# Kernel tuning notes

Measured on AMD Instinct MI355X. Metric: run time of the kernel, lower is better.

## Reference

```python
import jax, jax.numpy as jnp
import numpy as np

N, E = 50000, 800000
IN, EIN, HID, OUT = 128, 64, 64, 64
NEG_SLOPE = 0.2


def setup_inputs() -> dict:
    key = jax.random.key(0)
    ks = jax.random.split(key, 24)
    p = lambda k, shape: jax.random.normal(k, shape, jnp.float32) * 0.05
    return {
        'x': jax.random.normal(ks[0], (N, IN), jnp.float32),
        'edge_index': jax.random.randint(ks[1], (2, E), 0, N, jnp.int64),
        'edge_attr': jax.random.normal(ks[2], (E, EIN), jnp.float32),
        'batch': jnp.sort(jax.random.randint(ks[3], (N,), 0, 64, jnp.int64)),
        # GATConv 1 (in -> hidden, edge_dim=EIN)
        'W1': p(ks[4], (IN, HID)), 'a_src1': p(ks[5], (HID,)), 'a_dst1': p(ks[6], (HID,)),
        'We1': p(ks[7], (EIN, HID)), 'a_e1': p(ks[8], (HID,)), 'b1': jnp.zeros((HID,), jnp.float32),
        # GATConv 2 (hidden -> out)
        'W2': p(ks[9], (HID, OUT)), 'a_src2': p(ks[10], (OUT,)), 'a_dst2': p(ks[11], (OUT,)),
        'We2': p(ks[12], (EIN, OUT)), 'a_e2': p(ks[13], (OUT,)), 'b2': jnp.zeros((OUT,), jnp.float32),
        # edge MLP
        'Wm1': p(ks[14], (EIN, HID)), 'bm1': jnp.zeros((HID,), jnp.float32),
        'Wm2': p(ks[15], (HID, OUT)), 'bm2': jnp.zeros((OUT,), jnp.float32),
    }


def _gat(x, src, dst, edge_attr, W, a_s, a_d, We, a_e, b, n):
    # PyG GATConv (heads=1): add self-loops with edge_attr fill_value='mean'
    ones = jnp.ones((src.shape[0],), x.dtype)
    deg = jax.ops.segment_sum(ones, dst, num_segments=n)
    loop_attr = jax.ops.segment_sum(edge_attr, dst, num_segments=n) / jnp.maximum(deg, 1.0)[:, None]
    ar = jnp.arange(n)
    src2 = jnp.concatenate([src, ar])
    dst2 = jnp.concatenate([dst, ar])
    ea = jnp.concatenate([edge_attr, loop_attr], axis=0)  # [E+N, EIN]
    h = x @ W                                             # [N, C]
    a_src = h @ a_s                                       # [N]
    a_dst = h @ a_d                                       # [N]
    a_edge = (ea @ We) @ a_e                              # [E+N]
    alpha = jax.nn.leaky_relu(a_src[src2] + a_dst[dst2] + a_edge, NEG_SLOPE)
    # scatter-softmax over incoming edges of each dst node
    amax = jax.ops.segment_max(alpha, dst2, num_segments=n)
    ex = jnp.exp(alpha - amax[dst2])
    denom = jax.ops.segment_sum(ex, dst2, num_segments=n)
    coef = ex / denom[dst2]                               # [E+N]
    out = jax.ops.segment_sum(h[src2] * coef[:, None], dst2, num_segments=n)
    return out + b


def reference(x, edge_index, edge_attr, batch,
              W1, a_src1, a_dst1, We1, a_e1, b1,
              W2, a_src2, a_dst2, We2, a_e2, b2,
              Wm1, bm1, Wm2, bm2):
    n = x.shape[0]
    src, dst = edge_index[0], edge_index[1]
    h = _gat(x, src, dst, edge_attr, W1, a_src1, a_dst1, We1, a_e1, b1, n)
    h = jax.nn.elu(h)
    h = _gat(h, src, dst, edge_attr, W2, a_src2, a_dst2, We2, a_e2, b2, n)
    e = jax.nn.relu(edge_attr @ Wm1 + bm1) @ Wm2 + bm2
    return h, e, batch
```

## Files before the change

### kernel.cpp

```cpp
#include <hip/hip_runtime.h>

constexpr int NN = 50000;
constexpr int NE = 800000;
constexpr int C = 64;
constexpr int IN_DIM = 128;
constexpr float NEG = 0.2f;
constexpr int NB = (NN + 255) / 256;

typedef __attribute__((ext_vector_type(8))) short short8;
typedef __attribute__((ext_vector_type(4))) float f32x4;

__device__ __forceinline__ unsigned short f2bf(float f) {
    unsigned u = __float_as_uint(f);
    unsigned r = 0x7FFFu + ((u >> 16) & 1u);
    return (unsigned short)((u + r) >> 16);
}
__device__ __forceinline__ unsigned pack_bf2(float a, float b) {
    return (unsigned)f2bf(a) | ((unsigned)f2bf(b) << 16);
}

__global__ void k_vecs(const float* __restrict__ We1, const float* __restrict__ ae1v,
                       const float* __restrict__ We2, const float* __restrict__ ae2v,
                       const float* __restrict__ W1, const float* __restrict__ as1,
                       const float* __restrict__ ad1,
                       const float* __restrict__ W2, const float* __restrict__ as2,
                       const float* __restrict__ ad2,
                       float* __restrict__ out) {
    int t = blockIdx.x * blockDim.x + threadIdx.x;
    const float* M; const float* v; int row;
    if      (t < 64)  { M = We1; v = ae1v; row = t; }
    else if (t < 128) { M = We2; v = ae2v; row = t - 64; }
    else if (t < 256) { M = W1;  v = as1;  row = t - 128; }
    else if (t < 384) { M = W1;  v = ad1;  row = t - 256; }
    else if (t < 448) { M = W2;  v = as2;  row = t - 384; }
    else              { M = W2;  v = ad2;  row = t - 448; }
    float s = 0.f;
    #pragma unroll
    for (int c = 0; c < 64; ++c) s += M[row * 64 + c] * v[c];
    out[t] = s;
}

__global__ __launch_bounds__(256) void k_mlp_mfma(
        const float* __restrict__ ea,
        const float* __restrict__ Wm1, const float* __restrict__ bm1,
        const float* __restrict__ Wm2, const float* __restrict__ bm2,
        const float* __restrict__ wv,
        float* __restrict__ eout, float* __restrict__ ae1, float* __restrict__ ae2) {
    constexpr int AP = 144;
    __shared__ char Atile[128 * AP];
    __shared__ char Bt1[64 * AP];
    __shared__ char Bt2[64 * AP];
    const int t = threadIdx.x;
    const long long E0 = (long long)blockIdx.x * 128;
    const int l = t & 63;

    {
        const int j = t & 15;
        const int eb = t >> 4;
        float4 wk1 = *(const float4*)&wv[j * 4];
        float4 wk2 = *(const float4*)&wv[64 + j * 4];
        const float4* g = (const float4*)(ea + E0 * 64);
        float s1[8], s2[8];
        #pragma unroll
        for (int q = 0; q < 8; ++q) {
            float4 v = g[t + 256 * q];
            int e = eb + 16 * q;
            s1[q] = v.x * wk1.x + v.y * wk1.y + v.z * wk1.z + v.w * wk1.w;
            s2[q] = v.x * wk2.x + v.y * wk2.y + v.z * wk2.z + v.w * wk2.w;
            uint2 wr;
            wr.x = pack_bf2(v.x, v.y);
            wr.y = pack_bf2(v.z, v.w);
            *(uint2*)(Atile + e * AP + j * 8) = wr;
        }
        #pragma unroll
        for (int off = 1; off < 16; off <<= 1) {
            #pragma unroll
            for (int q = 0; q < 8; ++q) {
                s1[q] += __shfl_xor(s1[q], off);
                s2[q] += __shfl_xor(s2[q], off);
            }
        }
        float o1 = 0.f, o2 = 0.f;
        #pragma unroll
        for (int q = 0; q < 8; ++q) {
            if (j == q)     o1 = s1[q];
            if (j == q + 8) o2 = s2[q];
        }
        if (j < 8) ae1[E0 + eb + 16 * j] = o1;
        else       ae2[E0 + eb + 16 * (j - 8)] = o2;
    }
    {
        const int c = t & 63, kq = t >> 6;
        #pragma unroll
        for (int i = 0; i < 16; i += 2) {
            int k = kq * 16 + i;
            *(unsigned*)(Bt1 + c * AP + k * 2) = pack_bf2(Wm1[k * 64 + c], Wm1[(k + 1) * 64 + c]);
            *(unsigned*)(Bt2 + c * AP + k * 2) = pack_bf2(Wm2[k * 64 + c], Wm2[(k + 1) * 64 + c]);
        }
    }
    __syncthreads();

    const int m0 = (t >> 6) * 32;
    const int lr = l & 15;
    const int lk = (l >> 4) * 8;

    f32x4 acc[2][4] = {};
    #pragma unroll
    for (int ks = 0; ks < 2; ++ks) {
        int ko = ks * 32 + lk;
        short8 a0 = *(const short8*)(Atile + (m0 + lr) * AP + ko * 2);
        short8 a1 = *(const short8*)(Atile + (m0 + 16 + lr) * AP + ko * 2);
        #pragma unroll
        for (int nt = 0; nt < 4; ++nt) {
            short8 b = *(const short8*)(Bt1 + (nt * 16 + lr) * AP + ko * 2);
            acc[0][nt] = __builtin_amdgcn_mfma_f32_16x16x32_bf16(a0, b, acc[0][nt], 0, 0, 0);
            acc[1][nt] = __builtin_amdgcn_mfma_f32_16x16x32_bf16(a1, b, acc[1][nt], 0, 0, 0);
        }
    }
    {
        float b1v[4];
        #pragma unroll
        for (int nt = 0; nt < 4; ++nt) b1v[nt] = bm1[nt * 16 + lr];
        #pragma unroll
        for (int mt = 0; mt < 2; ++mt)
        #pragma unroll
        for (int nt = 0; nt < 4; ++nt)
        #pragma unroll
        for (int r = 0; r < 4; ++r) {
            int row = m0 + mt * 16 + (l >> 4) * 4 + r;
            int col = nt * 16 + lr;
            float v = fmaxf(acc[mt][nt][r] + b1v[nt], 0.f);
            *(unsigned short*)(Atile + row * AP + col * 2) = f2bf(v);
        }
    }
    f32x4 acc2[2][4] = {};
    #pragma unroll
    for (int ks = 0; ks < 2; ++ks) {
        int ko = ks * 32 + lk;
        short8 a0 = *(const short8*)(Atile + (m0 + lr) * AP + ko * 2);
        short8 a1 = *(const short8*)(Atile + (m0 + 16 + lr) * AP + ko * 2);
        #pragma unroll
        for (int nt = 0; nt < 4; ++nt) {
            short8 b = *(const short8*)(Bt2 + (nt * 16 + lr) * AP + ko * 2);
            acc2[0][nt] = __builtin_amdgcn_mfma_f32_16x16x32_bf16(a0, b, acc2[0][nt], 0, 0, 0);
            acc2[1][nt] = __builtin_amdgcn_mfma_f32_16x16x32_bf16(a1, b, acc2[1][nt], 0, 0, 0);
        }
    }
    {
        float b2v[4];
        #pragma unroll
        for (int nt = 0; nt < 4; ++nt) b2v[nt] = bm2[nt * 16 + lr];
        #pragma unroll
        for (int mt = 0; mt < 2; ++mt)
        #pragma unroll
        for (int nt = 0; nt < 4; ++nt)
        #pragma unroll
        for (int r = 0; r < 4; ++r) {
            int row = m0 + mt * 16 + (l >> 4) * 4 + r;
            eout[(E0 + row) * 64 + nt * 16 + lr] = acc2[mt][nt][r] + b2v[nt];
        }
    }
}

template <int K>
__global__ __launch_bounds__(256) void k_feat_mfma(
        const float* __restrict__ x, const float* __restrict__ W,
        const float* __restrict__ uv,
        float* __restrict__ h, float* __restrict__ asrc, float* __restrict__ adst,
        int M) {
    constexpr int AP = K * 2 + 16;
    constexpr int QW = K / 4;
    constexpr int NQ = K / 8;
    constexpr int EPQ = 256 / QW;
    __shared__ char Atile[128 * AP];
    __shared__ char Bt[64 * AP];
    const int t = threadIdx.x;
    const int M0 = blockIdx.x * 128;
    const int l = t & 63;

    {
        const int j = t % QW;
        const int eb = t / QW;
        float4 wk1 = *(const float4*)&uv[j * 4];
        float4 wk2 = *(const float4*)&uv[K + j * 4];
        const float4* g = (const float4*)(x + (long long)M0 * K);
        float s1[NQ], s2[NQ];
        #pragma unroll
        for (int q = 0; q < NQ; ++q) {
            int e = eb + EPQ * q;
            float4 v = make_float4(0.f, 0.f, 0.f, 0.f);
            if (M0 + e < M) v = g[t + 256 * q];
            s1[q] = v.x * wk1.x + v.y * wk1.y + v.z * wk1.z + v.w * wk1.w;
            s2[q] = v.x * wk2.x + v.y * wk2.y + v.z * wk2.z + v.w * wk2.w;
            uint2 wr;
            wr.x = pack_bf2(v.x, v.y);
            wr.y = pack_bf2(v.z, v.w);
            *(uint2*)(Atile + e * AP + j * 8) = wr;
        }
        #pragma unroll
        for (int off = 1; off < QW; off <<= 1) {
            #pragma unroll
            for (int q = 0; q < NQ; ++q) {
                s1[q] += __shfl_xor(s1[q], off);
                s2[q] += __shfl_xor(s2[q], off);
            }
        }
        float o1 = 0.f, o2 = 0.f;
        #pragma unroll
        for (int q = 0; q < NQ; ++q) {
            if (j == q)      o1 = s1[q];
            if (j == q + NQ) o2 = s2[q];
        }
        if (j < NQ) { int e = eb + EPQ * j;        if (M0 + e < M) asrc[M0 + e] = o1; }
        else        { int e = eb + EPQ * (j - NQ); if (M0 + e < M) adst[M0 + e] = o2; }
    }
    {
        const int c = t & 63, kq = t >> 6;
        #pragma unroll
        for (int i = 0; i < K / 4; i += 2) {
            int k = kq * (K / 4) + i;
            *(unsigned*)(Bt + c * AP + k * 2) = pack_bf2(W[k * 64 + c], W[(k + 1) * 64 + c]);
        }
    }
    __syncthreads();

    const int m0 = (t >> 6) * 32;
    const int lr = l & 15;
    const int lk = (l >> 4) * 8;

    f32x4 acc[2][4] = {};
    #pragma unroll
    for (int ks = 0; ks < K / 32; ++ks) {
        int ko = ks * 32 + lk;
        short8 a0 = *(const short8*)(Atile + (m0 + lr) * AP + ko * 2);
        short8 a1 = *(const short8*)(Atile + (m0 + 16 + lr) * AP + ko * 2);
        #pragma unroll
        for (int nt = 0; nt < 4; ++nt) {
            short8 b = *(const short8*)(Bt + (nt * 16 + lr) * AP + ko * 2);
            acc[0][nt] = __builtin_amdgcn_mfma_f32_16x16x32_bf16(a0, b, acc[0][nt], 0, 0, 0);
            acc[1][nt] = __builtin_amdgcn_mfma_f32_16x16x32_bf16(a1, b, acc[1][nt], 0, 0, 0);
        }
    }
    #pragma unroll
    for (int mt = 0; mt < 2; ++mt)
    #pragma unroll
    for (int nt = 0; nt < 4; ++nt)
    #pragma unroll
    for (int r = 0; r < 4; ++r) {
        int row = m0 + mt * 16 + (l >> 4) * 4 + r;
        if (M0 + row < M)
            h[(long long)(M0 + row) * 64 + nt * 16 + lr] = acc[mt][nt][r];
    }
}

__global__ void k_hist(const int* __restrict__ dst, int* __restrict__ hist) {
    int t = blockIdx.x * blockDim.x + threadIdx.x;
    if (t >= NE) return;
    atomicAdd(&hist[dst[t]], 1);
}

__global__ void k_scan1(const int* __restrict__ hist, int* __restrict__ row_ptr,
                        int* __restrict__ bsum) {
    __shared__ int s[256];
    int t = threadIdx.x;
    int idx = blockIdx.x * 256 + t;
    int v = (idx < NN) ? hist[idx] : 0;
    s[t] = v;
    __syncthreads();
    #pragma unroll
    for (int off = 1; off < 256; off <<= 1) {
        int x = (t >= off) ? s[t - off] : 0;
        __syncthreads();
        s[t] += x;
        __syncthreads();
    }
    if (idx < NN) row_ptr[idx] = s[t] - v;
    if (t == 255) bsum[blockIdx.x] = s[255];
}

__global__ void k_scan2(int* __restrict__ bsum) {
    __shared__ int s[256];
    int t = threadIdx.x;
    int v = (t < NB) ? bsum[t] : 0;
    s[t] = v;
    __syncthreads();
    #pragma unroll
    for (int off = 1; off < 256; off <<= 1) {
        int x = (t >= off) ? s[t - off] : 0;
        __syncthreads();
        s[t] += x;
        __syncthreads();
    }
    if (t < NB) bsum[t] = s[t] - v;
}

__global__ void k_scan3(const int* __restrict__ bsum, int* __restrict__ row_ptr,
                        int* __restrict__ cursor) {
    int idx = blockIdx.x * 256 + threadIdx.x;
    if (idx < NN) {
        int r = row_ptr[idx] + bsum[blockIdx.x];
        row_ptr[idx] = r;
        cursor[idx] = r;
    }
    if (idx == 0) row_ptr[NN] = NE;
}

__global__ void k_scatter(const int* __restrict__ src, const int* __restrict__ dst,
                          const float* __restrict__ ae1, const float* __restrict__ ae2,
                          int* __restrict__ cursor, float4* __restrict__ csr) {
    int t = blockIdx.x * blockDim.x + threadIdx.x;
    if (t >= NE) return;
    int d = dst[t];
    int pos = atomicAdd(&cursor[d], 1);
    csr[pos] = make_float4(__int_as_float(src[t]), ae1[t], ae2[t], 0.f);
}

template <bool IS_L1>
__global__ void k_gat(const int* __restrict__ row_ptr, const float4* __restrict__ csr,
                      const float* __restrict__ asrc, const float* __restrict__ adst,
                      const float* __restrict__ h, const float* __restrict__ bias,
                      float* __restrict__ out) {
    int n = blockIdx.x * 4 + (threadIdx.x >> 6);
    if (n >= NN) return;
    int lane = threadIdx.x & 63;
    int g = lane >> 4, s = lane & 15;
    int beg = row_ptr[n], end = row_ptr[n + 1];
    float adn = adst[n];
    float m = -1e30f, l = 0.f, sum_ae = 0.f;
    float4 acc = make_float4(0.f, 0.f, 0.f, 0.f);

    int i = beg + g;
    float4 rc = make_float4(0.f, 0.f, 0.f, 0.f);
    float4 hv = rc;
    float asv = 0.f;
    if (i < end) {
        rc = csr[i];
        int sr = __float_as_int(rc.x);
        hv = *(const float4*)&h[(long long)sr * 64 + s * 4];
        asv = asrc[sr];
    }
    for (; i < end; i += 4) {
        float4 rn = rc, hn = hv; float asn = asv;
        if (i + 4 < end) {
            rn = csr[i + 4];
            int sr2 = __float_as_int(rn.x);
            hn = *(const float4*)&h[(long long)sr2 * 64 + s * 4];
            asn = asrc[sr2];
        }
        float ae = IS_L1 ? rc.y : rc.z;
        sum_ae += ae;
        float a = asv + adn + ae;
        a = a > 0.f ? a : NEG * a;
        float mn = fmaxf(m, a);
        float sc = __expf(m - mn), p = __expf(a - mn);
        l = l * sc + p;
        acc.x = acc.x * sc + p * hv.x;
        acc.y = acc.y * sc + p * hv.y;
        acc.z = acc.z * sc + p * hv.z;
        acc.w = acc.w * sc + p * hv.w;
        m = mn;
        rc = rn; hv = hn; asv = asn;
    }
    #pragma unroll
    for (int off = 16; off < 64; off <<= 1) {
        float mo = __shfl_xor(m, off);
        float lo = __shfl_xor(l, off);
        float ax = __shfl_xor(acc.x, off);
        float ay = __shfl_xor(acc.y, off);
        float az = __shfl_xor(acc.z, off);
        float aw = __shfl_xor(acc.w, off);
        float so = __shfl_xor(sum_ae, off);
        float mn = fmaxf(m, mo);
        float s1 = __expf(m - mn), s2 = __expf(mo - mn);
        l = l * s1 + lo * s2;
        acc.x = acc.x * s1 + ax * s2;
        acc.y = acc.y * s1 + ay * s2;
        acc.z = acc.z * s1 + az * s2;
        acc.w = acc.w * s1 + aw * s2;
        sum_ae += so;
        m = mn;
    }
    {
        float deg = (float)(end - beg);
        float ae = sum_ae / fmaxf(deg, 1.f);
        float a = asrc[n] + adn + ae;
        a = a > 0.f ? a : NEG * a;
        float4 hvn = *(const float4*)&h[(long long)n * 64 + s * 4];
        float mn = fmaxf(m, a);
        float sc = __expf(m - mn), p = __expf(a - mn);
        l = l * sc + p;
        acc.x = acc.x * sc + p * hvn.x;
        acc.y = acc.y * sc + p * hvn.y;
        acc.z = acc.z * sc + p * hvn.z;
        acc.w = acc.w * sc + p * hvn.w;
    }
    if (g == 0) {
        float4 o;
        o.x = acc.x / l + bias[s * 4 + 0];
        o.y = acc.y / l + bias[s * 4 + 1];
        o.z = acc.z / l + bias[s * 4 + 2];
        o.w = acc.w / l + bias[s * 4 + 3];
        if (IS_L1) {
            o.x = o.x > 0.f ? o.x : expm1f(o.x);
            o.y = o.y > 0.f ? o.y : expm1f(o.y);
            o.z = o.z > 0.f ? o.z : expm1f(o.z);
            o.w = o.w > 0.f ? o.w : expm1f(o.w);
        }
        *(float4*)&out[(long long)n * 64 + s * 4] = o;
    }
}

__global__ void k_batch(const int* __restrict__ batch, float* __restrict__ out) {
    int t = blockIdx.x * blockDim.x + threadIdx.x;
    if (t >= NN) return;
    out[t] = (float)batch[t];
}

extern "C" void kernel_launch(void* const* d_in, const int* in_sizes, int n_in,
                              void* d_out, int out_size, void* d_ws, size_t ws_size,
                              hipStream_t stream) {
    const float* x     = (const float*)d_in[0];
    const int*   eidx  = (const int*)d_in[1];
    const float* eattr = (const float*)d_in[2];
    const int*   batch = (const int*)d_in[3];
    const float* W1 = (const float*)d_in[4];
    const float* as1 = (const float*)d_in[5];
    const float* ad1 = (const float*)d_in[6];
    const float* We1 = (const float*)d_in[7];
    const float* vae1 = (const float*)d_in[8];
    const float* b1  = (const float*)d_in[9];
    const float* W2 = (const float*)d_in[10];
    const float* as2 = (const float*)d_in[11];
    const float* ad2 = (const float*)d_in[12];
    const float* We2 = (const float*)d_in[13];
    const float* vae2 = (const float*)d_in[14];
    const float* b2  = (const float*)d_in[15];
    const float* Wm1 = (const float*)d_in[16];
    const float* bm1 = (const float*)d_in[17];
    const float* Wm2 = (const float*)d_in[18];
    const float* bm2 = (const float*)d_in[19];

    const int* src = eidx;
    const int* dst = eidx + NE;

    float* out_h = (float*)d_out;
    float* out_e = out_h + (long long)NN * C;
    float* out_b = out_e + (long long)NE * C;

    float4* csr   = (float4*)d_ws;
    float* ae1    = (float*)(csr + NE);
    float* ae2    = ae1 + NE;
    float* h      = ae2 + NE;
    float* out1   = h + (long long)NN * C;
    float* asrc   = out1 + (long long)NN * C;
    float* adst   = asrc + NN;
    float* vecs   = adst + NN;
    int*   hist   = (int*)(vecs + 512);
    int*   row_ptr= hist + NN;
    int*   cursor = row_ptr + NN + 1;
    int*   bsum   = cursor + NN;

    k_vecs<<<2, 256, 0, stream>>>(We1, vae1, We2, vae2, W1, as1, ad1, W2, as2, ad2, vecs);

    k_mlp_mfma<<<NE / 128, 256, 0, stream>>>(eattr, Wm1, bm1, Wm2, bm2, vecs,
                                             out_e, ae1, ae2);

    (void)hipMemsetAsync(hist, 0, sizeof(int) * NN, stream);
    k_hist<<<(NE + 255) / 256, 256, 0, stream>>>(dst, hist);
    k_scan1<<<NB, 256, 0, stream>>>(hist, row_ptr, bsum);
    k_scan2<<<1, 256, 0, stream>>>(bsum);
    k_scan3<<<NB, 256, 0, stream>>>(bsum, row_ptr, cursor);
    k_scatter<<<(NE + 255) / 256, 256, 0, stream>>>(src, dst, ae1, ae2, cursor, csr);

    k_feat_mfma<IN_DIM><<<(NN + 127) / 128, 256, 0, stream>>>(x, W1, vecs + 128,
                                                              h, asrc, adst, NN);
    k_gat<true><<<(NN + 3) / 4, 256, 0, stream>>>(row_ptr, csr, asrc, adst, h, b1, out1);

    k_feat_mfma<C><<<(NN + 127) / 128, 256, 0, stream>>>(out1, W2, vecs + 384,
                                                         h, asrc, adst, NN);
    k_gat<false><<<(NN + 3) / 4, 256, 0, stream>>>(row_ptr, csr, asrc, adst, h, b2, out_h);

    k_batch<<<(NN + 255) / 256, 256, 0, stream>>>(batch, out_b);
}
```

Before: 304.9 us.

## Store node features and CSR edge scores in bf16, fuse histogram into MLP

```diff
diff --git a/kernel.cpp b/kernel.cpp
--- a/kernel.cpp
+++ b/kernel.cpp
@@ -17,6 +17,9 @@
 }
 __device__ __forceinline__ unsigned pack_bf2(float a, float b) {
     return (unsigned)f2bf(a) | ((unsigned)f2bf(b) << 16);
+}
+__device__ __forceinline__ float bf2f(unsigned u) {
+    return __uint_as_float(u << 16);
 }
 
 __global__ void k_vecs(const float* __restrict__ We1, const float* __restrict__ ae1v,
@@ -41,11 +44,12 @@
 }
 
 __global__ __launch_bounds__(256) void k_mlp_mfma(
-        const float* __restrict__ ea,
+        const float* __restrict__ ea, const int* __restrict__ dst,
         const float* __restrict__ Wm1, const float* __restrict__ bm1,
         const float* __restrict__ Wm2, const float* __restrict__ bm2,
         const float* __restrict__ wv,
-        float* __restrict__ eout, float* __restrict__ ae1, float* __restrict__ ae2) {
+        float* __restrict__ eout, float* __restrict__ ae1, float* __restrict__ ae2,
+        int* __restrict__ hist) {
     constexpr int AP = 144;
     __shared__ char Atile[128 * AP];
     __shared__ char Bt1[64 * AP];
@@ -53,6 +57,8 @@
     const int t = threadIdx.x;
     const long long E0 = (long long)blockIdx.x * 128;
     const int l = t & 63;
+
+    if (t < 128) atomicAdd(&hist[dst[E0 + t]], 1);
 
     {
         const int j = t & 15;
@@ -166,8 +172,8 @@
 __global__ __launch_bounds__(256) void k_feat_mfma(
         const float* __restrict__ x, const float* __restrict__ W,
         const float* __restrict__ uv,
-        float* __restrict__ h, float* __restrict__ asrc, float* __restrict__ adst,
-        int M) {
+        unsigned short* __restrict__ h, float* __restrict__ asrc,
+        float* __restrict__ adst, int M) {
     constexpr int AP = K * 2 + 16;
     constexpr int QW = K / 4;
     constexpr int NQ = K / 8;
@@ -249,14 +255,8 @@
     for (int r = 0; r < 4; ++r) {
         int row = m0 + mt * 16 + (l >> 4) * 4 + r;
         if (M0 + row < M)
-            h[(long long)(M0 + row) * 64 + nt * 16 + lr] = acc[mt][nt][r];
-    }
-}
-
-__global__ void k_hist(const int* __restrict__ dst, int* __restrict__ hist) {
-    int t = blockIdx.x * blockDim.x + threadIdx.x;
-    if (t >= NE) return;
-    atomicAdd(&hist[dst[t]], 1);
+            h[(long long)(M0 + row) * 64 + nt * 16 + lr] = f2bf(acc[mt][nt][r]);
+    }
 }
 
 __global__ void k_scan1(const int* __restrict__ hist, int* __restrict__ row_ptr,
@@ -307,18 +307,18 @@
 
 __global__ void k_scatter(const int* __restrict__ src, const int* __restrict__ dst,
                           const float* __restrict__ ae1, const float* __restrict__ ae2,
-                          int* __restrict__ cursor, float4* __restrict__ csr) {
+                          int* __restrict__ cursor, uint2* __restrict__ csr) {
     int t = blockIdx.x * blockDim.x + threadIdx.x;
     if (t >= NE) return;
     int d = dst[t];
     int pos = atomicAdd(&cursor[d], 1);
-    csr[pos] = make_float4(__int_as_float(src[t]), ae1[t], ae2[t], 0.f);
+    csr[pos] = make_uint2((unsigned)src[t], pack_bf2(ae1[t], ae2[t]));
 }
 
 template <bool IS_L1>
-__global__ void k_gat(const int* __restrict__ row_ptr, const float4* __restrict__ csr,
+__global__ void k_gat(const int* __restrict__ row_ptr, const uint2* __restrict__ csr,
                       const float* __restrict__ asrc, const float* __restrict__ adst,
-                      const float* __restrict__ h, const float* __restrict__ bias,
+                      const unsigned short* __restrict__ h, const float* __restrict__ bias,
                       float* __restrict__ out) {
     int n = blockIdx.x * 4 + (threadIdx.x >> 6);
     if (n >= NN) return;
@@ -330,36 +330,34 @@
     float4 acc = make_float4(0.f, 0.f, 0.f, 0.f);
 
     int i = beg + g;
-    float4 rc = make_float4(0.f, 0.f, 0.f, 0.f);
-    float4 hv = rc;
+    uint2 rc = make_uint2(0u, 0u);
+    ushort4 hu = make_ushort4(0, 0, 0, 0);
     float asv = 0.f;
     if (i < end) {
         rc = csr[i];
-        int sr = __float_as_int(rc.x);
-        hv = *(const float4*)&h[(long long)sr * 64 + s * 4];
-        asv = asrc[sr];
+        hu = *(const ushort4*)&h[(long long)rc.x * 64 + s * 4];
+        asv = asrc[rc.x];
     }
     for (; i < end; i += 4) {
-        float4 rn = rc, hn = hv; float asn = asv;
+        uint2 rn = rc; ushort4 hn = hu; float asn = asv;
         if (i + 4 < end) {
             rn = csr[i + 4];
-            int sr2 = __float_as_int(rn.x);
-            hn = *(const float4*)&h[(long long)sr2 * 64 + s * 4];
-            asn = asrc[sr2];
-        }
-        float ae = IS_L1 ? rc.y : rc.z;
+            hn = *(const ushort4*)&h[(long long)rn.x * 64 + s * 4];
+            asn = asrc[rn.x];
+        }
+        float ae = IS_L1 ? bf2f(rc.y & 0xFFFFu) : bf2f(rc.y >> 16);
         sum_ae += ae;
         float a = asv + adn + ae;
         a = a > 0.f ? a : NEG * a;
         float mn = fmaxf(m, a);
         float sc = __expf(m - mn), p = __expf(a - mn);
         l = l * sc + p;
-        acc.x = acc.x * sc + p * hv.x;
-        acc.y = acc.y * sc + p * hv.y;
-        acc.z = acc.z * sc + p * hv.z;
-        acc.w = acc.w * sc + p * hv.w;
+        acc.x = acc.x * sc + p * bf2f(hu.x);
+        acc.y = acc.y * sc + p * bf2f(hu.y);
+        acc.z = acc.z * sc + p * bf2f(hu.z);
+        acc.w = acc.w * sc + p * bf2f(hu.w);
         m = mn;
-        rc = rn; hv = hn; asv = asn;
+        rc = rn; hu = hn; asv = asn;
     }
     #pragma unroll
     for (int off = 16; off < 64; off <<= 1) {
@@ -385,14 +383,14 @@
         float ae = sum_ae / fmaxf(deg, 1.f);
         float a = asrc[n] + adn + ae;
         a = a > 0.f ? a : NEG * a;
-        float4 hvn = *(const float4*)&h[(long long)n * 64 + s * 4];
+        ushort4 hun = *(const ushort4*)&h[(long long)n * 64 + s * 4];
         float mn = fmaxf(m, a);
         float sc = __expf(m - mn), p = __expf(a - mn);
         l = l * sc + p;
-        acc.x = acc.x * sc + p * hvn.x;
-        acc.y = acc.y * sc + p * hvn.y;
-        acc.z = acc.z * sc + p * hvn.z;
-        acc.w = acc.w * sc + p * hvn.w;
+        acc.x = acc.x * sc + p * bf2f(hun.x);
+        acc.y = acc.y * sc + p * bf2f(hun.y);
+        acc.z = acc.z * sc + p * bf2f(hun.z);
+        acc.w = acc.w * sc + p * bf2f(hun.w);
     }
     if (g == 0) {
         float4 o;
@@ -447,12 +445,12 @@
     float* out_e = out_h + (long long)NN * C;
     float* out_b = out_e + (long long)NE * C;
 
-    float4* csr   = (float4*)d_ws;
+    uint2* csr    = (uint2*)d_ws;
     float* ae1    = (float*)(csr + NE);
     float* ae2    = ae1 + NE;
-    float* h      = ae2 + NE;
-    float* out1   = h + (long long)NN * C;
-    float* asrc   = out1 + (long long)NN * C;
+    float* out1   = ae2 + NE;
+    unsigned short* h = (unsigned short*)(out1 + (long long)NN * C);
+    float* asrc   = (float*)(h + (long long)NN * C);
     float* adst   = asrc + NN;
     float* vecs   = adst + NN;
     int*   hist   = (int*)(vecs + 512);
@@ -460,13 +458,13 @@
     int*   cursor = row_ptr + NN + 1;
     int*   bsum   = cursor + NN;
 
+    (void)hipMemsetAsync(hist, 0, sizeof(int) * NN, stream);
+
     k_vecs<<<2, 256, 0, stream>>>(We1, vae1, We2, vae2, W1, as1, ad1, W2, as2, ad2, vecs);
 
-    k_mlp_mfma<<<NE / 128, 256, 0, stream>>>(eattr, Wm1, bm1, Wm2, bm2, vecs,
-                                             out_e, ae1, ae2);
-
-    (void)hipMemsetAsync(hist, 0, sizeof(int) * NN, stream);
-    k_hist<<<(NE + 255) / 256, 256, 0, stream>>>(dst, hist);
+    k_mlp_mfma<<<NE / 128, 256, 0, stream>>>(eattr, dst, Wm1, bm1, Wm2, bm2, vecs,
+                                             out_e, ae1, ae2, hist);
+
     k_scan1<<<NB, 256, 0, stream>>>(hist, row_ptr, bsum);
     k_scan2<<<1, 256, 0, stream>>>(bsum);
     k_scan3<<<NB, 256, 0, stream>>>(bsum, row_ptr, cursor);
```

New measurement: 277.6 us. 9.0% less time.
